# Performance work log

Measured on AMD Instinct MI355X. Metric: run time of the kernel, lower is better.

The kernel has to match this reference:

```python
import jax, jax.numpy as jnp
import numpy as np

NX, NY, NZ = 432, 496, 1   # grid_size (nx, ny, nz), nz must be 1
NBEV = 128                 # NUM_BEV_FEATURES
K = 4                      # NUM_K
SHRINK = 0.0025            # SHRINK_TH
BN_EPS = 1e-3


def setup_inputs():
    key = jax.random.key(0)
    ks = jax.random.split(key, 8)
    B, P, NPT, D, M = 2, 6000, 4096, 64, 1024
    pillar_features = jax.random.normal(ks[0], (B, P, D), jnp.float32)
    point_features = jax.random.normal(ks[1], (B, NPT, D), jnp.float32)
    # unique flat BEV cells per scene -> coords columns (z, y, x) as in OpenPCDet coords[:,1:4]
    coords = []
    for b in range(B):
        flat = jax.random.permutation(jax.random.fold_in(ks[2], b), NX * NY)[:P]
        y = flat // NX
        x = flat % NX
        z = jnp.zeros_like(flat)
        coords.append(jnp.stack([z, y, x], axis=1))
    voxel_coords = jnp.stack(coords, 0).astype(jnp.int32)
    adapt_w = jax.random.normal(ks[3], (NBEV // 2, D * K), jnp.float32) * 0.05  # Linear(no bias)
    mem_w = jax.random.normal(ks[4], (M, D), jnp.float32) * 0.05               # MemoryUnit slots
    bn_gamma = jnp.ones((NBEV // 2,), jnp.float32)
    bn_beta = jnp.zeros((NBEV // 2,), jnp.float32)
    return dict(pillar_features=pillar_features, point_features=point_features,
                voxel_coords=voxel_coords, adapt_w=adapt_w, mem_w=mem_w,
                bn_gamma=bn_gamma, bn_beta=bn_beta)


def _forward(pillar_features, point_features, voxel_coords, adapt_w, mem_w, bn_gamma, bn_beta):
    def per_batch(pillars, points, coords):
        # pillars [P,D], points [Np,D], coords [P,3] = (z, y, x)
        # get_score: softmax over points dim, top-k points per pillar
        score = jax.nn.softmax(pillars @ points.T, axis=1)            # [P,Np]
        _, idx = jax.lax.top_k(score, K)                              # [P,K] (indices detached)
        pts = points[idx]                                             # [P,K,D]
        # MemoryUnit (MemAE-style): softmax attention over memory, hard-shrink-relu, L1 renorm
        x = pts.reshape(-1, points.shape[1])                          # [P*K,D]
        att = jax.nn.softmax(x @ mem_w.T, axis=1)                     # [P*K,M]
        shr = jax.nn.relu(att - SHRINK) * att / (jnp.abs(att - SHRINK) + 1e-12)
        att = shr / (jnp.sum(jnp.abs(shr), axis=1, keepdims=True) + 1e-12)
        mem_out = (att @ mem_w).reshape(pillars.shape[0], -1)         # [P, K*D]
        # adapt_layer (Linear, no bias) -> BatchNorm1d (training stats over pillars) -> ReLU
        h = mem_out @ adapt_w.T                                       # [P, NBEV//2]
        mu = jnp.mean(h, axis=0)
        var = jnp.var(h, axis=0)
        h = (h - mu) / jnp.sqrt(var + BN_EPS) * bn_gamma + bn_beta
        h = jax.nn.relu(h)
        feats = jnp.concatenate([pillars, h], axis=1)                 # [P, NBEV]
        # scatter into dense BEV grid: index = z + y*nx + x (nz==1 so z==0)
        flat = coords[:, 0] + coords[:, 1] * NX + coords[:, 2]
        spatial = jnp.zeros((NBEV, NZ * NX * NY), feats.dtype).at[:, flat].set(feats.T)
        pind = jnp.zeros((3, NZ * NX * NY), feats.dtype)
        pind = pind.at[0, flat].set(coords[:, 1].astype(feats.dtype))
        pind = pind.at[1, flat].set(coords[:, 2].astype(feats.dtype))
        pind = pind.at[2, flat].set(coords[:, 0].astype(feats.dtype))
        return spatial, pind

    spatial, pind = jax.vmap(per_batch)(pillar_features, point_features, voxel_coords)
    B = spatial.shape[0]
    return spatial.reshape(B, NBEV * NZ, NY, NX), pind.reshape(B, 3 * NZ, NY, NX)


def reference(pillar_features, point_features, voxel_coords, adapt_w, mem_w, bn_gamma, bn_beta):
    return _forward(pillar_features, point_features, voxel_coords, adapt_w, mem_w, bn_gamma, bn_beta)
```

## Files before the change

### kernel.cpp

```cpp
#include <hip/hip_runtime.h>

#define NXg 432
#define NYg 496
#define SCELLS (NXg*NYg)
#define PB 6000
#define NPTS 4096
#define DD 64
#define MM 1024
#define KK 4
#define BB 2
#define NROWS (PB*KK)
#define NSEG 16
#define SEGPTS (NPTS/NSEG)
#define CHROWS 64
#define NCHNK (SEGPTS/CHROWS)
#define MOP 6
#define SHRINK_TH 0.0025f
#define BN_EPS 1e-3f
#define NEG_INF -3.402823466e38f

#define INS4(v, id, v0,v1,v2,v3, i0,i1,i2,i3) { \
    bool g0 = (v) > v0, g1 = (v) > v1, g2 = (v) > v2; \
    v3 = g2 ? v2 : (v);              i3 = g2 ? i2 : (id); \
    v2 = g2 ? (g1 ? v1 : (v)) : v2;  i2 = g2 ? (g1 ? i1 : (id)) : i2; \
    v1 = g1 ? (g0 ? v0 : (v)) : v1;  i1 = g1 ? (g0 ? i0 : (id)) : i1; \
    v0 = g0 ? (v) : v0;              i0 = g0 ? (id) : i0; \
}

__global__ __launch_bounds__(256) void k_init_inv(int* __restrict__ inv) {
    int i = blockIdx.x*256 + threadIdx.x;
    inv[i] = -1;
}

__global__ __launch_bounds__(256) void k_scatter_inv(const int* __restrict__ coords,
                                                     int* __restrict__ inv) {
    int i = blockIdx.x*256 + threadIdx.x;
    if (i >= BB*PB) return;
    int b = i / PB, p = i % PB;
    const int* c = coords + (size_t)i*3;
    int flat = c[0] + c[1]*NXg + c[2];
    inv[b*SCELLS + flat] = p;
}

__global__ __launch_bounds__(256) void k_score_topk(const float* __restrict__ pillars,
                                                    const float* __restrict__ points,
                                                    float* __restrict__ pV,
                                                    int* __restrict__ pI) {
    __shared__ float4 sPt[CHROWS*16];
    const int b = blockIdx.y;
    const int seg = blockIdx.z;
    const int t = threadIdx.x;
    const int pillar = blockIdx.x*256 + t;
    const int prow = pillar < PB ? pillar : PB-1;
    const int j0 = seg * SEGPTS;

    const float4* pil4  = (const float4*)pillars;
    const float4* ptsB4 = (const float4*)(points + (size_t)b*NPTS*DD);

    float4 wreg[16];
    #pragma unroll
    for (int d4 = 0; d4 < 16; d4++)
        wreg[d4] = pil4[((size_t)b*PB + prow)*16 + d4];

    float tv0=NEG_INF, tv1=NEG_INF, tv2=NEG_INF, tv3=NEG_INF;
    int   ti0=0, ti1=0, ti2=0, ti3=0;

    for (int ch = 0; ch < NCHNK; ch++) {
        const float4* src = ptsB4 + (size_t)(j0 + ch*CHROWS)*16;
        for (int i = t; i < CHROWS*16; i += 256)
            sPt[i] = src[i];
        __syncthreads();

        const int jb = j0 + ch*CHROWS;
        for (int j = 0; j < CHROWS; j += 2) {
            float a0 = 0.f, a1 = 0.f;
            #pragma unroll
            for (int d4 = 0; d4 < 16; d4++) {
                float4 x0 = sPt[j*16 + d4];
                float4 x1 = sPt[(j+1)*16 + d4];
                a0 += wreg[d4].x*x0.x + wreg[d4].y*x0.y + wreg[d4].z*x0.z + wreg[d4].w*x0.w;
                a1 += wreg[d4].x*x1.x + wreg[d4].y*x1.y + wreg[d4].z*x1.z + wreg[d4].w*x1.w;
            }
            if (a0 > tv3) INS4(a0, jb+j,   tv0,tv1,tv2,tv3, ti0,ti1,ti2,ti3)
            if (a1 > tv3) INS4(a1, jb+j+1, tv0,tv1,tv2,tv3, ti0,ti1,ti2,ti3)
        }
        __syncthreads();
    }

    if (pillar < PB) {
        size_t ob = (((size_t)b*NSEG + seg)*PB + pillar)*KK;
        pV[ob+0]=tv0; pV[ob+1]=tv1; pV[ob+2]=tv2; pV[ob+3]=tv3;
        pI[ob+0]=ti0; pI[ob+1]=ti1; pI[ob+2]=ti2; pI[ob+3]=ti3;
    }
}

__global__ __launch_bounds__(256) void k_merge(const float* __restrict__ pV,
                                               const int* __restrict__ pI,
                                               int* __restrict__ idxOut) {
    int i = blockIdx.x*256 + threadIdx.x;
    if (i >= BB*PB) return;
    int b = i / PB, p = i % PB;
    float fv0=NEG_INF, fv1=NEG_INF, fv2=NEG_INF, fv3=NEG_INF;
    int fi0=0, fi1=0, fi2=0, fi3=0;
    for (int s = 0; s < NSEG; s++) {
        size_t base = (((size_t)b*NSEG + s)*PB + p)*KK;
        #pragma unroll
        for (int q = 0; q < 4; q++) {
            float v = pV[base+q];
            if (v > fv3) INS4(v, pI[base+q], fv0,fv1,fv2,fv3, fi0,fi1,fi2,fi3)
        }
    }
    idxOut[(size_t)i*KK+0]=fi0; idxOut[(size_t)i*KK+1]=fi1;
    idxOut[(size_t)i*KK+2]=fi2; idxOut[(size_t)i*KK+3]=fi3;
}

__global__ __launch_bounds__(256) void k_logits(const float* __restrict__ points,
                                                const int* __restrict__ idxIn,
                                                const float* __restrict__ memw,
                                                float* __restrict__ logits,
                                                int b) {
    __shared__ float4 sX4[64*16];
    __shared__ int sId[64];
    const int t = threadIdx.x;
    const int lane = t & 63, wv = t >> 6;
    const int row0 = blockIdx.x * 64;
    const int cg = blockIdx.y * 256 + wv * 64;

    if (t < 64) sId[t] = idxIn[(size_t)b*NROWS + row0 + t];

    const float4* mw4 = (const float4*)memw;
    float4 wreg[16];
    #pragma unroll
    for (int d4 = 0; d4 < 16; d4++) wreg[d4] = mw4[(size_t)(cg + lane)*16 + d4];

    __syncthreads();
    const float4* ptsB4 = (const float4*)(points + (size_t)b*NPTS*DD);
    for (int i = t; i < 1024; i += 256) {
        int r = i >> 4, c = i & 15;
        sX4[i] = ptsB4[(size_t)sId[r]*16 + c];
    }
    __syncthreads();

    for (int r = 0; r < 64; r += 2) {
        float a0 = 0.f, a1 = 0.f;
        #pragma unroll
        for (int d4 = 0; d4 < 16; d4++) {
            float4 x0 = sX4[r*16 + d4];
            float4 x1 = sX4[(r+1)*16 + d4];
            a0 += wreg[d4].x*x0.x + wreg[d4].y*x0.y + wreg[d4].z*x0.z + wreg[d4].w*x0.w;
            a1 += wreg[d4].x*x1.x + wreg[d4].y*x1.y + wreg[d4].z*x1.z + wreg[d4].w*x1.w;
        }
        logits[(size_t)(row0 + r)*MM + cg + lane] = a0;
        logits[(size_t)(row0 + r + 1)*MM + cg + lane] = a1;
    }
}

__global__ __launch_bounds__(256) void k_moG(const float* __restrict__ logits,
                                             const float* __restrict__ memw,
                                             float* __restrict__ mo,
                                             int b) {
    __shared__ __align__(16) char smem[22528];
    float4* sAtt4 = (float4*)smem;
    float4* sW4   = (float4*)(smem + 6144);
    float*  sWf   = (float*)sW4;
    __shared__ float sM[24], sRinv[24], sRsc[24];
    const int t = threadIdx.x;
    const int lane = t & 63, wv = t >> 6;
    const int p0 = blockIdx.x * MOP;
    const int row0 = p0 * 4;

    const float4* lg4 = (const float4*)logits;
    #pragma unroll
    for (int rr = 0; rr < MOP; rr++) {
        int r = wv*MOP + rr;
        size_t base = (size_t)(row0 + r)*256;
        float4 l0 = lg4[base + lane];
        float4 l1 = lg4[base + 64 + lane];
        float4 l2 = lg4[base + 128 + lane];
        float4 l3 = lg4[base + 192 + lane];
        float m = fmaxf(fmaxf(fmaxf(l0.x,l0.y),fmaxf(l0.z,l0.w)),
                 fmaxf(fmaxf(fmaxf(l1.x,l1.y),fmaxf(l1.z,l1.w)),
                 fmaxf(fmaxf(fmaxf(l2.x,l2.y),fmaxf(l2.z,l2.w)),
                       fmaxf(fmaxf(l3.x,l3.y),fmaxf(l3.z,l3.w)))));
        #pragma unroll
        for (int off = 1; off < 64; off <<= 1) m = fmaxf(m, __shfl_xor(m, off));
        l0.x=__expf(l0.x-m); l0.y=__expf(l0.y-m); l0.z=__expf(l0.z-m); l0.w=__expf(l0.w-m);
        l1.x=__expf(l1.x-m); l1.y=__expf(l1.y-m); l1.z=__expf(l1.z-m); l1.w=__expf(l1.w-m);
        l2.x=__expf(l2.x-m); l2.y=__expf(l2.y-m); l2.z=__expf(l2.z-m); l2.w=__expf(l2.w-m);
        l3.x=__expf(l3.x-m); l3.y=__expf(l3.y-m); l3.z=__expf(l3.z-m); l3.w=__expf(l3.w-m);
        float s = (l0.x+l0.y+l0.z+l0.w) + (l1.x+l1.y+l1.z+l1.w)
                + (l2.x+l2.y+l2.z+l2.w) + (l3.x+l3.y+l3.z+l3.w);
        #pragma unroll
        for (int off = 1; off < 64; off <<= 1) s += __shfl_xor(s, off);
        float rinv = 1.f / s;
        float sh = 0.f;
        {
            float e, tt;
            e=l0.x*rinv; tt=e-SHRINK_TH; sh += tt>0.f ? e*tt/(tt+1e-12f) : 0.f;
            e=l0.y*rinv; tt=e-SHRINK_TH; sh += tt>0.f ? e*tt/(tt+1e-12f) : 0.f;
            e=l0.z*rinv; tt=e-SHRINK_TH; sh += tt>0.f ? e*tt/(tt+1e-12f) : 0.f;
            e=l0.w*rinv; tt=e-SHRINK_TH; sh += tt>0.f ? e*tt/(tt+1e-12f) : 0.f;
            e=l1.x*rinv; tt=e-SHRINK_TH; sh += tt>0.f ? e*tt/(tt+1e-12f) : 0.f;
            e=l1.y*rinv; tt=e-SHRINK_TH; sh += tt>0.f ? e*tt/(tt+1e-12f) : 0.f;
            e=l1.z*rinv; tt=e-SHRINK_TH; sh += tt>0.f ? e*tt/(tt+1e-12f) : 0.f;
            e=l1.w*rinv; tt=e-SHRINK_TH; sh += tt>0.f ? e*tt/(tt+1e-12f) : 0.f;
            e=l2.x*rinv; tt=e-SHRINK_TH; sh += tt>0.f ? e*tt/(tt+1e-12f) : 0.f;
            e=l2.y*rinv; tt=e-SHRINK_TH; sh += tt>0.f ? e*tt/(tt+1e-12f) : 0.f;
            e=l2.z*rinv; tt=e-SHRINK_TH; sh += tt>0.f ? e*tt/(tt+1e-12f) : 0.f;
            e=l2.w*rinv; tt=e-SHRINK_TH; sh += tt>0.f ? e*tt/(tt+1e-12f) : 0.f;
            e=l3.x*rinv; tt=e-SHRINK_TH; sh += tt>0.f ? e*tt/(tt+1e-12f) : 0.f;
            e=l3.y*rinv; tt=e-SHRINK_TH; sh += tt>0.f ? e*tt/(tt+1e-12f) : 0.f;
            e=l3.z*rinv; tt=e-SHRINK_TH; sh += tt>0.f ? e*tt/(tt+1e-12f) : 0.f;
            e=l3.w*rinv; tt=e-SHRINK_TH; sh += tt>0.f ? e*tt/(tt+1e-12f) : 0.f;
        }
        #pragma unroll
        for (int off = 1; off < 64; off <<= 1) sh += __shfl_xor(sh, off);
        if (lane == 0) { sM[r] = m; sRinv[r] = rinv; sRsc[r] = 1.f/(sh + 1e-12f); }
    }
    __syncthreads();

    float acc[MOP];
    #pragma unroll
    for (int s=0;s<MOP;s++) acc[s]=0.f;
    const float4* mw4 = (const float4*)memw;

    for (int tile = 0; tile < 16; tile++) {
        __syncthreads();
        for (int i = t; i < 24*16; i += 256) {
            int rr = i >> 4, m4 = i & 15;
            float4 lg = lg4[(size_t)(row0 + rr)*256 + tile*16 + m4];
            float m = sM[rr], rinv = sRinv[rr], rsc = sRsc[rr];
            float4 o;
            float e, tt;
            e=__expf(lg.x-m)*rinv; tt=e-SHRINK_TH; o.x = (tt>0.f ? e*tt/(tt+1e-12f) : 0.f)*rsc;
            e=__expf(lg.y-m)*rinv; tt=e-SHRINK_TH; o.y = (tt>0.f ? e*tt/(tt+1e-12f) : 0.f)*rsc;
            e=__expf(lg.z-m)*rinv; tt=e-SHRINK_TH; o.z = (tt>0.f ? e*tt/(tt+1e-12f) : 0.f)*rsc;
            e=__expf(lg.w-m)*rinv; tt=e-SHRINK_TH; o.w = (tt>0.f ? e*tt/(tt+1e-12f) : 0.f)*rsc;
            sAtt4[rr*16 + m4] = o;
        }
        #pragma unroll 4
        for (int i = t; i < 1024; i += 256) {
            int m = i >> 4, c4 = i & 15;
            sW4[m*16 + c4] = mw4[(size_t)(tile*64 + m)*16 + c4];
        }
        __syncthreads();
        #pragma unroll 4
        for (int m4 = 0; m4 < 16; m4++) {
            float w0 = sWf[(m4*4+0)*64 + lane];
            float w1 = sWf[(m4*4+1)*64 + lane];
            float w2 = sWf[(m4*4+2)*64 + lane];
            float w3 = sWf[(m4*4+3)*64 + lane];
            #pragma unroll
            for (int s = 0; s < MOP; s++) {
                float4 a4 = sAtt4[(wv + 4*s)*16 + m4];
                acc[s] += a4.x*w0 + a4.y*w1 + a4.z*w2 + a4.w*w3;
            }
        }
    }
    #pragma unroll
    for (int s = 0; s < MOP; s++) {
        int r = wv + 4*s;
        mo[(size_t)(p0 + (r >> 2))*256 + (r & 3)*64 + lane] = acc[s];
    }
}

__global__ __launch_bounds__(256) void k_adapt(const float* __restrict__ mo,
                                               const float* __restrict__ adaptw,
                                               float* __restrict__ hOut,
                                               int b) {
    __shared__ float4 sMo4[12*64];
    const int t = threadIdx.x;
    const int lane = t & 63, wv = t >> 6;
    const int p0 = blockIdx.x * 12;

    const float4* mo4 = (const float4*)(mo + (size_t)p0*256);
    #pragma unroll
    for (int q = 0; q < 3; q++)
        sMo4[q*256 + t] = mo4[q*256 + t];
    __syncthreads();

    const float4* adG4 = (const float4*)adaptw;
    float h0 = 0.f, h1 = 0.f, h2 = 0.f;
    #pragma unroll
    for (int qt = 0; qt < 4; qt++) {
        float4 wreg[16];
        #pragma unroll
        for (int i = 0; i < 16; i++)
            wreg[i] = adG4[(size_t)lane*64 + qt*16 + i];
        #pragma unroll
        for (int i = 0; i < 16; i++) {
            float4 q0 = sMo4[(wv+0)*64 + qt*16 + i];
            float4 q1 = sMo4[(wv+4)*64 + qt*16 + i];
            float4 q2 = sMo4[(wv+8)*64 + qt*16 + i];
            h0 += wreg[i].x*q0.x + wreg[i].y*q0.y + wreg[i].z*q0.z + wreg[i].w*q0.w;
            h1 += wreg[i].x*q1.x + wreg[i].y*q1.y + wreg[i].z*q1.z + wreg[i].w*q1.w;
            h2 += wreg[i].x*q2.x + wreg[i].y*q2.y + wreg[i].z*q2.z + wreg[i].w*q2.w;
        }
    }
    hOut[((size_t)b*PB + p0 + wv + 0)*DD + lane] = h0;
    hOut[((size_t)b*PB + p0 + wv + 4)*DD + lane] = h1;
    hOut[((size_t)b*PB + p0 + wv + 8)*DD + lane] = h2;
}

__global__ __launch_bounds__(256) void k_bn1(const float* __restrict__ h,
                                             float* __restrict__ pSum,
                                             float* __restrict__ pSq) {
    const int bid = blockIdx.x;
    const int b = bid >> 5, ch = bid & 31;
    const int r0 = ch*188;
    int r1 = r0 + 188; if (r1 > PB) r1 = PB;
    __shared__ float sS[4*64], sS2[4*64];
    const int t = threadIdx.x;
    const int c = t & 63, stripe = t >> 6;
    float s = 0.f, s2 = 0.f;
    for (int r = r0 + stripe; r < r1; r += 4) {
        float v = h[((size_t)b*PB + r)*DD + c];
        s += v; s2 += v*v;
    }
    sS[stripe*64 + c] = s; sS2[stripe*64 + c] = s2;
    __syncthreads();
    if (t < 64) {
        float ts = sS[t] + sS[64+t] + sS[128+t] + sS[192+t];
        float ts2 = sS2[t] + sS2[64+t] + sS2[128+t] + sS2[192+t];
        pSum[(size_t)bid*64 + t] = ts;
        pSq[(size_t)bid*64 + t] = ts2;
    }
}

__global__ __launch_bounds__(64) void k_bn2(const float* __restrict__ pSum,
                                            const float* __restrict__ pSq,
                                            const float* __restrict__ gamma,
                                            float* __restrict__ bnMu,
                                            float* __restrict__ bnScale) {
    const int b = blockIdx.x;
    const int t = threadIdx.x;
    float ts = 0.f, ts2 = 0.f;
    for (int ch = 0; ch < 32; ch++) {
        ts += pSum[(size_t)(b*32 + ch)*64 + t];
        ts2 += pSq[(size_t)(b*32 + ch)*64 + t];
    }
    float mu = ts / (float)PB;
    float var = ts2 / (float)PB - mu*mu;
    if (var < 0.f) var = 0.f;
    bnMu[b*64+t] = mu;
    bnScale[b*64+t] = gamma[t] / sqrtf(var + BN_EPS);
}

__global__ __launch_bounds__(256) void k_fill(const int* __restrict__ inv,
                                              const float* __restrict__ pillars,
                                              const float* __restrict__ h,
                                              const float* __restrict__ bnMu,
                                              const float* __restrict__ bnScale,
                                              const float* __restrict__ beta,
                                              float* __restrict__ out) {
    const int b = blockIdx.y;
    const int f = blockIdx.x*256 + threadIdx.x;
    __shared__ float sMu[64], sSc[64], sBe[64];
    if (threadIdx.x < 64) {
        sMu[threadIdx.x] = bnMu[b*64+threadIdx.x];
        sSc[threadIdx.x] = bnScale[b*64+threadIdx.x];
        sBe[threadIdx.x] = beta[threadIdx.x];
    }
    __syncthreads();
    int iv = inv[b*SCELLS + f];
    bool occ = iv >= 0;
    int iv0 = occ ? iv : 0;
    float* sp = out + (size_t)b*128*SCELLS;
    const float* prow = pillars + ((size_t)b*PB + iv0)*DD;
    const float* hrow = h + ((size_t)b*PB + iv0)*DD;
    #pragma unroll 4
    for (int c = 0; c < 64; c++)
        sp[(size_t)c*SCELLS + f] = occ ? prow[c] : 0.f;
    #pragma unroll 4
    for (int c = 0; c < 64; c++) {
        float v = 0.f;
        if (occ) {
            float hv = hrow[c];
            v = fmaxf((hv - sMu[c])*sSc[c] + sBe[c], 0.f);
        }
        sp[(size_t)(64+c)*SCELLS + f] = v;
    }
    float* pi = out + (size_t)BB*128*SCELLS + (size_t)b*3*SCELLS;
    pi[f]              = occ ? (float)(f / NXg) : 0.f;
    pi[SCELLS + f]     = occ ? (float)(f % NXg) : 0.f;
    pi[2*(size_t)SCELLS + f] = 0.f;
}

extern "C" void kernel_launch(void* const* d_in, const int* in_sizes, int n_in,
                              void* d_out, int out_size, void* d_ws, size_t ws_size,
                              hipStream_t stream) {
    const float* pillars = (const float*)d_in[0];
    const float* points  = (const float*)d_in[1];
    const int*   coords  = (const int*)d_in[2];
    const float* adaptw  = (const float*)d_in[3];
    const float* memw    = (const float*)d_in[4];
    const float* gamma   = (const float*)d_in[5];
    const float* beta    = (const float*)d_in[6];
    float* out = (float*)d_out;

    char* w = (char*)d_ws;
    int* inv = (int*)w;        w += (size_t)BB*SCELLS*4;
    int* idx = (int*)w;        w += (size_t)BB*PB*KK*4;
    float* h = (float*)w;      w += (size_t)BB*PB*DD*4;
    float* bnMu = (float*)w;   w += (size_t)BB*64*4;
    float* bnScale = (float*)w; w += (size_t)BB*64*4;
    float* pSum = (float*)w;   w += (size_t)BB*32*64*4;
    float* pSq = (float*)w;    w += (size_t)BB*32*64*4;
    float* mo = (float*)w;     w += (size_t)PB*256*4;
    float* logits = (float*)w;
    float* pV = logits;
    int*   pI = (int*)(logits + (size_t)BB*NSEG*PB*KK);

    k_init_inv<<<dim3(BB*SCELLS/256), dim3(256), 0, stream>>>(inv);
    k_scatter_inv<<<dim3((BB*PB+255)/256), dim3(256), 0, stream>>>(coords, inv);
    k_score_topk<<<dim3((PB+255)/256, BB, NSEG), dim3(256), 0, stream>>>(pillars, points, pV, pI);
    k_merge<<<dim3((BB*PB+255)/256), dim3(256), 0, stream>>>(pV, pI, idx);
    for (int b = 0; b < BB; b++) {
        k_logits<<<dim3(NROWS/64, 4), dim3(256), 0, stream>>>(points, idx, memw, logits, b);
        k_moG<<<dim3(PB/MOP), dim3(256), 0, stream>>>(logits, memw, mo, b);
        k_adapt<<<dim3(PB/12), dim3(256), 0, stream>>>(mo, adaptw, h, b);
    }
    k_bn1<<<dim3(BB*32), dim3(256), 0, stream>>>(h, pSum, pSq);
    k_bn2<<<dim3(BB), dim3(64), 0, stream>>>(pSum, pSq, gamma, bnMu, bnScale);
    k_fill<<<dim3(SCELLS/256, BB), dim3(256), 0, stream>>>(inv, pillars, h, bnMu, bnScale, beta, out);
}
```

Baseline: 775.1 us.

## Split memory-attention kernel into row-stats pass and register-tiled attention GEMM

```diff
diff --git a/kernel.cpp b/kernel.cpp
--- a/kernel.cpp
+++ b/kernel.cpp
@@ -14,7 +14,7 @@
 #define SEGPTS (NPTS/NSEG)
 #define CHROWS 64
 #define NCHNK (SEGPTS/CHROWS)
-#define MOP 6
+#define AR 32
 #define SHRINK_TH 0.0025f
 #define BN_EPS 1e-3f
 #define NEG_INF -3.402823466e38f
@@ -155,113 +155,126 @@
     }
 }
 
-__global__ __launch_bounds__(256) void k_moG(const float* __restrict__ logits,
-                                             const float* __restrict__ memw,
-                                             float* __restrict__ mo,
-                                             int b) {
-    __shared__ __align__(16) char smem[22528];
-    float4* sAtt4 = (float4*)smem;
-    float4* sW4   = (float4*)(smem + 6144);
-    float*  sWf   = (float*)sW4;
-    __shared__ float sM[24], sRinv[24], sRsc[24];
-    const int t = threadIdx.x;
-    const int lane = t & 63, wv = t >> 6;
-    const int p0 = blockIdx.x * MOP;
-    const int row0 = p0 * 4;
-
+__global__ __launch_bounds__(256) void k_stats(const float* __restrict__ logits,
+                                               float* __restrict__ stats,
+                                               int b) {
+    const int wv = threadIdx.x >> 6, lane = threadIdx.x & 63;
+    const int row = blockIdx.x*4 + wv;
     const float4* lg4 = (const float4*)logits;
-    #pragma unroll
-    for (int rr = 0; rr < MOP; rr++) {
-        int r = wv*MOP + rr;
-        size_t base = (size_t)(row0 + r)*256;
-        float4 l0 = lg4[base + lane];
-        float4 l1 = lg4[base + 64 + lane];
-        float4 l2 = lg4[base + 128 + lane];
-        float4 l3 = lg4[base + 192 + lane];
-        float m = fmaxf(fmaxf(fmaxf(l0.x,l0.y),fmaxf(l0.z,l0.w)),
-                 fmaxf(fmaxf(fmaxf(l1.x,l1.y),fmaxf(l1.z,l1.w)),
-                 fmaxf(fmaxf(fmaxf(l2.x,l2.y),fmaxf(l2.z,l2.w)),
-                       fmaxf(fmaxf(l3.x,l3.y),fmaxf(l3.z,l3.w)))));
-        #pragma unroll
-        for (int off = 1; off < 64; off <<= 1) m = fmaxf(m, __shfl_xor(m, off));
-        l0.x=__expf(l0.x-m); l0.y=__expf(l0.y-m); l0.z=__expf(l0.z-m); l0.w=__expf(l0.w-m);
-        l1.x=__expf(l1.x-m); l1.y=__expf(l1.y-m); l1.z=__expf(l1.z-m); l1.w=__expf(l1.w-m);
-        l2.x=__expf(l2.x-m); l2.y=__expf(l2.y-m); l2.z=__expf(l2.z-m); l2.w=__expf(l2.w-m);
-        l3.x=__expf(l3.x-m); l3.y=__expf(l3.y-m); l3.z=__expf(l3.z-m); l3.w=__expf(l3.w-m);
-        float s = (l0.x+l0.y+l0.z+l0.w) + (l1.x+l1.y+l1.z+l1.w)
-                + (l2.x+l2.y+l2.z+l2.w) + (l3.x+l3.y+l3.z+l3.w);
-        #pragma unroll
-        for (int off = 1; off < 64; off <<= 1) s += __shfl_xor(s, off);
-        float rinv = 1.f / s;
-        float sh = 0.f;
-        {
-            float e, tt;
-            e=l0.x*rinv; tt=e-SHRINK_TH; sh += tt>0.f ? e*tt/(tt+1e-12f) : 0.f;
-            e=l0.y*rinv; tt=e-SHRINK_TH; sh += tt>0.f ? e*tt/(tt+1e-12f) : 0.f;
-            e=l0.z*rinv; tt=e-SHRINK_TH; sh += tt>0.f ? e*tt/(tt+1e-12f) : 0.f;
-            e=l0.w*rinv; tt=e-SHRINK_TH; sh += tt>0.f ? e*tt/(tt+1e-12f) : 0.f;
-            e=l1.x*rinv; tt=e-SHRINK_TH; sh += tt>0.f ? e*tt/(tt+1e-12f) : 0.f;
-            e=l1.y*rinv; tt=e-SHRINK_TH; sh += tt>0.f ? e*tt/(tt+1e-12f) : 0.f;
-            e=l1.z*rinv; tt=e-SHRINK_TH; sh += tt>0.f ? e*tt/(tt+1e-12f) : 0.f;
-            e=l1.w*rinv; tt=e-SHRINK_TH; sh += tt>0.f ? e*tt/(tt+1e-12f) : 0.f;
-            e=l2.x*rinv; tt=e-SHRINK_TH; sh += tt>0.f ? e*tt/(tt+1e-12f) : 0.f;
-            e=l2.y*rinv; tt=e-SHRINK_TH; sh += tt>0.f ? e*tt/(tt+1e-12f) : 0.f;
-            e=l2.z*rinv; tt=e-SHRINK_TH; sh += tt>0.f ? e*tt/(tt+1e-12f) : 0.f;
-            e=l2.w*rinv; tt=e-SHRINK_TH; sh += tt>0.f ? e*tt/(tt+1e-12f) : 0.f;
-            e=l3.x*rinv; tt=e-SHRINK_TH; sh += tt>0.f ? e*tt/(tt+1e-12f) : 0.f;
-            e=l3.y*rinv; tt=e-SHRINK_TH; sh += tt>0.f ? e*tt/(tt+1e-12f) : 0.f;
-            e=l3.z*rinv; tt=e-SHRINK_TH; sh += tt>0.f ? e*tt/(tt+1e-12f) : 0.f;
-            e=l3.w*rinv; tt=e-SHRINK_TH; sh += tt>0.f ? e*tt/(tt+1e-12f) : 0.f;
-        }
-        #pragma unroll
-        for (int off = 1; off < 64; off <<= 1) sh += __shfl_xor(sh, off);
-        if (lane == 0) { sM[r] = m; sRinv[r] = rinv; sRsc[r] = 1.f/(sh + 1e-12f); }
-    }
-    __syncthreads();
-
-    float acc[MOP];
-    #pragma unroll
-    for (int s=0;s<MOP;s++) acc[s]=0.f;
+    size_t base = (size_t)row*256;
+    float4 l0 = lg4[base + lane];
+    float4 l1 = lg4[base + 64 + lane];
+    float4 l2 = lg4[base + 128 + lane];
+    float4 l3 = lg4[base + 192 + lane];
+    float m = fmaxf(fmaxf(fmaxf(l0.x,l0.y),fmaxf(l0.z,l0.w)),
+             fmaxf(fmaxf(fmaxf(l1.x,l1.y),fmaxf(l1.z,l1.w)),
+             fmaxf(fmaxf(fmaxf(l2.x,l2.y),fmaxf(l2.z,l2.w)),
+                   fmaxf(fmaxf(l3.x,l3.y),fmaxf(l3.z,l3.w)))));
+    #pragma unroll
+    for (int off = 1; off < 64; off <<= 1) m = fmaxf(m, __shfl_xor(m, off));
+    l0.x=__expf(l0.x-m); l0.y=__expf(l0.y-m); l0.z=__expf(l0.z-m); l0.w=__expf(l0.w-m);
+    l1.x=__expf(l1.x-m); l1.y=__expf(l1.y-m); l1.z=__expf(l1.z-m); l1.w=__expf(l1.w-m);
+    l2.x=__expf(l2.x-m); l2.y=__expf(l2.y-m); l2.z=__expf(l2.z-m); l2.w=__expf(l2.w-m);
+    l3.x=__expf(l3.x-m); l3.y=__expf(l3.y-m); l3.z=__expf(l3.z-m); l3.w=__expf(l3.w-m);
+    float s = (l0.x+l0.y+l0.z+l0.w) + (l1.x+l1.y+l1.z+l1.w)
+            + (l2.x+l2.y+l2.z+l2.w) + (l3.x+l3.y+l3.z+l3.w);
+    #pragma unroll
+    for (int off = 1; off < 64; off <<= 1) s += __shfl_xor(s, off);
+    float rinv = 1.f / s;
+    float sh = 0.f;
+    {
+        float e, tt;
+        e=l0.x*rinv; tt=e-SHRINK_TH; sh += tt>0.f ? e*tt/(tt+1e-12f) : 0.f;
+        e=l0.y*rinv; tt=e-SHRINK_TH; sh += tt>0.f ? e*tt/(tt+1e-12f) : 0.f;
+        e=l0.z*rinv; tt=e-SHRINK_TH; sh += tt>0.f ? e*tt/(tt+1e-12f) : 0.f;
+        e=l0.w*rinv; tt=e-SHRINK_TH; sh += tt>0.f ? e*tt/(tt+1e-12f) : 0.f;
+        e=l1.x*rinv; tt=e-SHRINK_TH; sh += tt>0.f ? e*tt/(tt+1e-12f) : 0.f;
+        e=l1.y*rinv; tt=e-SHRINK_TH; sh += tt>0.f ? e*tt/(tt+1e-12f) : 0.f;
+        e=l1.z*rinv; tt=e-SHRINK_TH; sh += tt>0.f ? e*tt/(tt+1e-12f) : 0.f;
+        e=l1.w*rinv; tt=e-SHRINK_TH; sh += tt>0.f ? e*tt/(tt+1e-12f) : 0.f;
+        e=l2.x*rinv; tt=e-SHRINK_TH; sh += tt>0.f ? e*tt/(tt+1e-12f) : 0.f;
+        e=l2.y*rinv; tt=e-SHRINK_TH; sh += tt>0.f ? e*tt/(tt+1e-12f) : 0.f;
+        e=l2.z*rinv; tt=e-SHRINK_TH; sh += tt>0.f ? e*tt/(tt+1e-12f) : 0.f;
+        e=l2.w*rinv; tt=e-SHRINK_TH; sh += tt>0.f ? e*tt/(tt+1e-12f) : 0.f;
+        e=l3.x*rinv; tt=e-SHRINK_TH; sh += tt>0.f ? e*tt/(tt+1e-12f) : 0.f;
+        e=l3.y*rinv; tt=e-SHRINK_TH; sh += tt>0.f ? e*tt/(tt+1e-12f) : 0.f;
+        e=l3.z*rinv; tt=e-SHRINK_TH; sh += tt>0.f ? e*tt/(tt+1e-12f) : 0.f;
+        e=l3.w*rinv; tt=e-SHRINK_TH; sh += tt>0.f ? e*tt/(tt+1e-12f) : 0.f;
+    }
+    #pragma unroll
+    for (int off = 1; off < 64; off <<= 1) sh += __shfl_xor(sh, off);
+    if (lane == 0) {
+        float4* st4 = (float4*)stats;
+        st4[(size_t)b*NROWS + row] = make_float4(m, rinv, 1.f/(sh + 1e-12f), 0.f);
+    }
+}
+
+__global__ __launch_bounds__(256) void k_attg(const float* __restrict__ logits,
+                                              const float* __restrict__ memw,
+                                              const float* __restrict__ stats,
+                                              float* __restrict__ mo,
+                                              int b) {
+    __shared__ __align__(16) float sAtt[AR*68];
+    __shared__ __align__(16) float4 sW4[64*16];
+    __shared__ float sSt[AR*4];
+    const int t = threadIdx.x;
+    const int cg = t & 15, rg = t >> 4;
+    const int row0 = blockIdx.x * AR;
+
+    if (t < AR) {
+        const float4* st4 = (const float4*)stats;
+        float4 s = st4[(size_t)b*NROWS + row0 + t];
+        sSt[t*4+0]=s.x; sSt[t*4+1]=s.y; sSt[t*4+2]=s.z; sSt[t*4+3]=s.w;
+    }
+    __syncthreads();
+
+    const float4* lg4 = (const float4*)logits;
     const float4* mw4 = (const float4*)memw;
+    float4 acc0 = make_float4(0.f,0.f,0.f,0.f);
+    float4 acc1 = make_float4(0.f,0.f,0.f,0.f);
 
     for (int tile = 0; tile < 16; tile++) {
-        __syncthreads();
-        for (int i = t; i < 24*16; i += 256) {
-            int rr = i >> 4, m4 = i & 15;
-            float4 lg = lg4[(size_t)(row0 + rr)*256 + tile*16 + m4];
-            float m = sM[rr], rinv = sRinv[rr], rsc = sRsc[rr];
-            float4 o;
-            float e, tt;
-            e=__expf(lg.x-m)*rinv; tt=e-SHRINK_TH; o.x = (tt>0.f ? e*tt/(tt+1e-12f) : 0.f)*rsc;
-            e=__expf(lg.y-m)*rinv; tt=e-SHRINK_TH; o.y = (tt>0.f ? e*tt/(tt+1e-12f) : 0.f)*rsc;
-            e=__expf(lg.z-m)*rinv; tt=e-SHRINK_TH; o.z = (tt>0.f ? e*tt/(tt+1e-12f) : 0.f)*rsc;
-            e=__expf(lg.w-m)*rinv; tt=e-SHRINK_TH; o.w = (tt>0.f ? e*tt/(tt+1e-12f) : 0.f)*rsc;
-            sAtt4[rr*16 + m4] = o;
-        }
-        #pragma unroll 4
-        for (int i = t; i < 1024; i += 256) {
-            int m = i >> 4, c4 = i & 15;
-            sW4[m*16 + c4] = mw4[(size_t)(tile*64 + m)*16 + c4];
+        #pragma unroll
+        for (int q = 0; q < 2; q++) {
+            int idx = q*256 + t;
+            int row = idx >> 4, m4 = idx & 15;
+            float4 lg = lg4[(size_t)(row0 + row)*256 + tile*16 + m4];
+            float m = sSt[row*4], rinv = sSt[row*4+1], rsc = sSt[row*4+2];
+            float4 o; float e, tt;
+            e=__expf(lg.x-m)*rinv; tt=e-SHRINK_TH; o.x=(tt>0.f?e*tt/(tt+1e-12f):0.f)*rsc;
+            e=__expf(lg.y-m)*rinv; tt=e-SHRINK_TH; o.y=(tt>0.f?e*tt/(tt+1e-12f):0.f)*rsc;
+            e=__expf(lg.z-m)*rinv; tt=e-SHRINK_TH; o.z=(tt>0.f?e*tt/(tt+1e-12f):0.f)*rsc;
+            e=__expf(lg.w-m)*rinv; tt=e-SHRINK_TH; o.w=(tt>0.f?e*tt/(tt+1e-12f):0.f)*rsc;
+            *(float4*)(sAtt + row*68 + m4*4) = o;
+        }
+        #pragma unroll
+        for (int q = 0; q < 4; q++) {
+            int idx = q*256 + t;
+            sW4[idx] = mw4[(size_t)tile*1024 + idx];
         }
         __syncthreads();
         #pragma unroll 4
         for (int m4 = 0; m4 < 16; m4++) {
-            float w0 = sWf[(m4*4+0)*64 + lane];
-            float w1 = sWf[(m4*4+1)*64 + lane];
-            float w2 = sWf[(m4*4+2)*64 + lane];
-            float w3 = sWf[(m4*4+3)*64 + lane];
-            #pragma unroll
-            for (int s = 0; s < MOP; s++) {
-                float4 a4 = sAtt4[(wv + 4*s)*16 + m4];
-                acc[s] += a4.x*w0 + a4.y*w1 + a4.z*w2 + a4.w*w3;
-            }
-        }
-    }
-    #pragma unroll
-    for (int s = 0; s < MOP; s++) {
-        int r = wv + 4*s;
-        mo[(size_t)(p0 + (r >> 2))*256 + (r & 3)*64 + lane] = acc[s];
-    }
+            float4 a0 = *(const float4*)(sAtt + (rg*2+0)*68 + m4*4);
+            float4 a1 = *(const float4*)(sAtt + (rg*2+1)*68 + m4*4);
+            float4 w0 = sW4[(m4*4+0)*16 + cg];
+            float4 w1 = sW4[(m4*4+1)*16 + cg];
+            float4 w2 = sW4[(m4*4+2)*16 + cg];
+            float4 w3 = sW4[(m4*4+3)*16 + cg];
+            acc0.x += a0.x*w0.x + a0.y*w1.x + a0.z*w2.x + a0.w*w3.x;
+            acc0.y += a0.x*w0.y + a0.y*w1.y + a0.z*w2.y + a0.w*w3.y;
+            acc0.z += a0.x*w0.z + a0.y*w1.z + a0.z*w2.z + a0.w*w3.z;
+            acc0.w += a0.x*w0.w + a0.y*w1.w + a0.z*w2.w + a0.w*w3.w;
+            acc1.x += a1.x*w0.x + a1.y*w1.x + a1.z*w2.x + a1.w*w3.x;
+            acc1.y += a1.x*w0.y + a1.y*w1.y + a1.z*w2.y + a1.w*w3.y;
+            acc1.z += a1.x*w0.z + a1.y*w1.z + a1.z*w2.z + a1.w*w3.z;
+            acc1.w += a1.x*w0.w + a1.y*w1.w + a1.z*w2.w + a1.w*w3.w;
+        }
+        __syncthreads();
+    }
+
+    *(float4*)(mo + (size_t)(row0 + rg*2 + 0)*64 + cg*4) = acc0;
+    *(float4*)(mo + (size_t)(row0 + rg*2 + 1)*64 + cg*4) = acc1;
 }
 
 __global__ __launch_bounds__(256) void k_adapt(const float* __restrict__ mo,
@@ -406,7 +419,8 @@
     float* bnScale = (float*)w; w += (size_t)BB*64*4;
     float* pSum = (float*)w;   w += (size_t)BB*32*64*4;
     float* pSq = (float*)w;    w += (size_t)BB*32*64*4;
-    float* mo = (float*)w;     w += (size_t)PB*256*4;
+    float* stats = (float*)w;  w += (size_t)BB*NROWS*4*4;
+    float* mo = (float*)w;     w += (size_t)NROWS*DD*4;
     float* logits = (float*)w;
     float* pV = logits;
     int*   pI = (int*)(logits + (size_t)BB*NSEG*PB*KK);
@@ -417,7 +431,8 @@
     k_merge<<<dim3((BB*PB+255)/256), dim3(256), 0, stream>>>(pV, pI, idx);
     for (int b = 0; b < BB; b++) {
         k_logits<<<dim3(NROWS/64, 4), dim3(256), 0, stream>>>(points, idx, memw, logits, b);
-        k_moG<<<dim3(PB/MOP), dim3(256), 0, stream>>>(logits, memw, mo, b);
+        k_stats<<<dim3(NROWS/4), dim3(256), 0, stream>>>(logits, stats, b);
+        k_attg<<<dim3(NROWS/AR), dim3(256), 0, stream>>>(logits, memw, stats, mo, b);
         k_adapt<<<dim3(PB/12), dim3(256), 0, stream>>>(mo, adaptw, h, b);
     }
     k_bn1<<<dim3(BB*32), dim3(256), 0, stream>>>(h, pSum, pSq);
```

New measurement: 627.4 us (median of 2 runs). 19.1% less time.
